# Performance work log

Measured on AMD Instinct MI355X. Metric: run time of the kernel, lower is better.

## Reference

```python
import jax, jax.numpy as jnp
import numpy as np

B, S, H, K, V = 1024, 50, 128, 4, 100000
ROUTING_TIMES = 3

def _squash(c):
    # c: [B,K,1,H]
    cap_norm = jnp.sum(jnp.square(c), -1, keepdims=True)
    scalar_factor = cap_norm / (1.0 + cap_norm) / jnp.sqrt(cap_norm + 1e-9)
    return scalar_factor * c

def setup_inputs() -> dict:
    key = jax.random.key(0)
    k1, k2, k3, k4, k5, k6 = jax.random.split(key, 6)
    item_seq = jax.random.randint(k1, (B, S), 0, V)
    mask = jax.random.randint(k2, (B, S), 0, 2).astype(jnp.float32)
    item = jax.random.randint(k3, (B, 1), 0, V)
    emb = jax.random.normal(k4, (V, H), dtype=jnp.float32) * 0.02
    W = jax.random.normal(k5, (H, H), dtype=jnp.float32) * (1.0 / np.sqrt(H))
    # bilinear_type==0 -> capsule routing logits initialized with randn
    capsule_weight0 = jax.random.normal(k6, (B, K, S), dtype=jnp.float32)
    return {"item_seq": item_seq, "mask": mask, "item": item,
            "emb": emb, "W": W, "capsule_weight0": capsule_weight0}

def reference(item_seq, mask, item, emb, W, capsule_weight0):
    # padding_idx=0: lookups see a zeroed row 0 (and get no grad there),
    # but calculate_loss uses the raw weight matrix.
    emb_lookup = emb.at[0].set(0.0)
    seq_emb = emb_lookup[item_seq]          # [B,S,H]
    item_e = emb_lookup[item[:, 0]]         # [B,H]  (squeeze(1))

    # CapsuleNetwork, bilinear_type==0: Linear(H,H,no bias) then repeat_interleave along hidden
    h = seq_emb @ W.T                        # [B,S,H]
    hat = jnp.repeat(h, K, axis=2)           # [B,S,H*K] (repeat_interleave semantics)
    hat = hat.reshape(B, S, K, H).transpose(0, 2, 1, 3)  # [B,K,S,H]
    hat_iter = jax.lax.stop_gradient(hat)    # stop_grad=True (detach)

    atten_mask = jnp.broadcast_to(mask[:, None, :], (B, K, S))
    cw = capsule_weight0
    cap = None
    for i in range(ROUTING_TIMES):
        # torch F.softmax with no dim on a 3-D tensor uses dim=0 (batch axis) -- faithful
        sw = jax.nn.softmax(cw, axis=0)
        sw = jnp.where(atten_mask == 0, 0.0, sw)[:, :, None, :]  # [B,K,1,S]
        src = hat_iter if i < ROUTING_TIMES - 1 else hat
        cap = _squash(sw @ src)                                   # [B,K,1,H]
        if i < ROUTING_TIMES - 1:
            delta = (hat_iter @ jnp.swapaxes(cap, 3, 2)).reshape(B, K, S)
            cw = cw + delta

    user_emb = cap.reshape(B, K, H)          # multi_interest_emb

    # hard readout: pick interest with max dot against target item
    cos = jnp.einsum('bkh,bh->bk', user_emb, item_e)
    k_index = jnp.argmax(cos, axis=1)        # [B]
    best = jnp.take_along_axis(user_emb, k_index[:, None, None], axis=1)[:, 0]  # [B,H]

    # cross-entropy over all items (raw embedding weight)
    scores = best @ emb.T                    # [B,V]
    logp = jax.nn.log_softmax(scores, axis=-1)
    loss = -jnp.mean(jnp.take_along_axis(logp, item, axis=1))
    return user_emb, loss
```

## Files before the change

kernel.cpp:

```cpp
#include <hip/hip_runtime.h>
#include <math.h>

#define BB 1024
#define SS 50
#define SSP 51
#define HH 128
#define KK 4
#define VV 100000
#define NVT 782
#define NVT8 784
#define KS (KK*SS)
#define NHM 400
#define NPAD_LAST 96.0f

typedef __attribute__((ext_vector_type(8))) short bf16x8;
typedef __attribute__((ext_vector_type(4))) float f32x4;

__device__ __forceinline__ ushort f2bf(float x) {
  unsigned u = __float_as_uint(x);
  unsigned r = u + 0x7FFF + ((u >> 16) & 1);
  return (ushort)(r >> 16);
}
__device__ __forceinline__ float bf2f(ushort u) {
  return __uint_as_float(((unsigned)u) << 16);
}
__device__ __forceinline__ bf16x8 cvt8(float4 a, float4 b) {
  bf16x8 r;
  r[0] = (short)f2bf(a.x); r[1] = (short)f2bf(a.y);
  r[2] = (short)f2bf(a.z); r[3] = (short)f2bf(a.w);
  r[4] = (short)f2bf(b.x); r[5] = (short)f2bf(b.y);
  r[6] = (short)f2bf(b.z); r[7] = (short)f2bf(b.w);
  return r;
}

__global__ __launch_bounds__(256) void k_pre(const float* __restrict__ emb,
                                             const float* __restrict__ cw0,
                                             float* __restrict__ cm,
                                             float* __restrict__ s1,
                                             float* __restrict__ s2,
                                             float* __restrict__ accum,
                                             const int* __restrict__ item_seq,
                                             const float* __restrict__ W,
                                             ushort* __restrict__ hb16) {
  const int t = threadIdx.x;
  if (blockIdx.x < NHM) {
    __shared__ __align__(16) ushort sWf[32 * 512];
    const int w = t >> 6;
    const int lane = t & 63;
    const int lr = lane & 15;
    const int lq = lane >> 4;
    const int m0 = blockIdx.x * 128;

#pragma unroll
    for (int it = 0; it < 8; ++it) {
      int pos = t + it * 256;
      int ch = pos >> 6, l = pos & 63;
      int n = (ch & 7) * 16 + (l & 15);
      int k0 = (ch >> 3) * 32 + (l >> 4) * 8;
      float4 a = *(const float4*)&W[n * HH + k0];
      float4 b = *(const float4*)&W[n * HH + k0 + 4];
      *(bf16x8*)&sWf[ch * 512 + l * 8] = cvt8(a, b);
    }

    bf16x8 af[4][2];
#pragma unroll
    for (int vv = 0; vv < 2; ++vv) {
      int m = m0 + w * 32 + vv * 16 + lr;
      int idx = item_seq[m];
#pragma unroll
      for (int ks = 0; ks < 4; ++ks) {
        if (idx != 0) {
          float4 a = *(const float4*)&emb[(size_t)idx * HH + ks * 32 + lq * 8];
          float4 b = *(const float4*)&emb[(size_t)idx * HH + ks * 32 + lq * 8 + 4];
          af[ks][vv] = cvt8(a, b);
        } else {
          af[ks][vv] = (bf16x8){0, 0, 0, 0, 0, 0, 0, 0};
        }
      }
    }
    __syncthreads();

    f32x4 acc[8][2];
#pragma unroll
    for (int nt = 0; nt < 8; ++nt)
#pragma unroll
      for (int vv = 0; vv < 2; ++vv) acc[nt][vv] = (f32x4){0.f, 0.f, 0.f, 0.f};

#pragma unroll
    for (int ks = 0; ks < 4; ++ks) {
      bf16x8 bw[8];
#pragma unroll
      for (int nt = 0; nt < 8; ++nt)
        bw[nt] = *(const bf16x8*)&sWf[(ks * 8 + nt) * 512 + lane * 8];
#pragma unroll
      for (int nt = 0; nt < 8; ++nt)
#pragma unroll
        for (int vv = 0; vv < 2; ++vv)
          acc[nt][vv] = __builtin_amdgcn_mfma_f32_16x16x32_bf16(af[ks][vv], bw[nt], acc[nt][vv], 0, 0, 0);
    }

#pragma unroll
    for (int nt = 0; nt < 8; ++nt)
#pragma unroll
      for (int vv = 0; vv < 2; ++vv)
#pragma unroll
        for (int r = 0; r < 4; ++r) {
          int m = m0 + w * 32 + vv * 16 + lq * 4 + r;
          hb16[(size_t)m * HH + nt * 16 + lr] = f2bf(acc[nt][vv][r]);
        }
  } else {
    __shared__ float red[256];
    const int c = blockIdx.x - NHM;
    if (t < 8) s1[t * KS + c] = 0.f;
    if (t >= 8 && t < 16) s2[(t - 8) * KS + c] = 0.f;
    if (c < 4) accum[c * 256 + t] = 0.f;
    float s = 0.f;
    for (int b = t; b < BB; b += 256) s += __expf(cw0[(size_t)b * KS + c]);
    red[t] = s;
    __syncthreads();
    for (int o = 128; o > 0; o >>= 1) {
      if (t < o) red[t] += red[t + o];
      __syncthreads();
    }
    if (t == 0) cm[c] = red[0];
  }
}

__global__ __launch_bounds__(256) void k_route(const float* __restrict__ cwsrc,
                                               float* __restrict__ cwdst,
                                               const ushort* __restrict__ hb16,
                                               const float* __restrict__ csum,
                                               int nslots,
                                               const float* __restrict__ mask,
                                               int last,
                                               float* __restrict__ out_ue,
                                               const float* __restrict__ emb,
                                               const int* __restrict__ item,
                                               ushort* __restrict__ bestb,
                                               float* __restrict__ csnext,
                                               float* __restrict__ si) {
  __shared__ ushort shT[128 * SSP];
  __shared__ float swl[KS];
  __shared__ float c32p[256];
  __shared__ float c32[128];
  __shared__ float csq[128];
  __shared__ float ie4r[32];
  __shared__ float ie4z[32];
  __shared__ float fac[4];
  __shared__ float cosk[4];
  __shared__ float cosr[4];
  __shared__ int kb;
  const int t = threadIdx.x;
  const int b = blockIdx.x;

  for (int p = t; p < (SS * HH) / 4; p += 256) {
    int flat = 4 * p;
    int s = flat >> 7, col = flat & 127;
    ushort4 v = *(const ushort4*)&hb16[(size_t)b * SS * HH + flat];
    shT[(col + 0) * SSP + s] = v.x;
    shT[(col + 1) * SSP + s] = v.y;
    shT[(col + 2) * SSP + s] = v.z;
    shT[(col + 3) * SSP + s] = v.w;
  }
  if (t < KS) {
    float den = 0.f;
    for (int g2 = 0; g2 < nslots; ++g2) den += csum[g2 * KS + t];
    float v = __expf(cwsrc[(size_t)b * KS + t]) / den;
    if (mask[b * SS + (t % SS)] == 0.0f) v = 0.0f;
    swl[t] = v;
  }
  __syncthreads();

  {
    int col = t & 127;
    int half = t >> 7;
    int k = col >> 5;
    float acc = 0.f;
    const float* swk = &swl[k * SS + half * 25];
    const ushort* hc = &shT[col * SSP + half * 25];
    for (int s = 0; s < 25; ++s) acc += swk[s] * bf2f(hc[s]);
    c32p[t] = acc;
  }
  __syncthreads();
  if (t < 128) c32[t] = c32p[t] + c32p[t + 128];
  __syncthreads();
  if (t < 4) {
    float nrm = 0.f;
#pragma unroll
    for (int j = 0; j < 32; ++j) { float c = c32[32 * t + j]; nrm += c * c; }
    nrm *= 4.0f;
    fac[t] = nrm / (1.0f + nrm) / sqrtf(nrm + 1e-9f);
  }
  __syncthreads();
  if (t < 128) csq[t] = c32[t] * fac[t >> 5];
  __syncthreads();

  if (!last) {
    if (t < KS) {
      int k = t / SS, s = t % SS;
      const float* cq = &csq[32 * k];
      float d = 0.f;
#pragma unroll
      for (int j = 0; j < 32; ++j) d += bf2f(shT[(32 * k + j) * SSP + s]) * cq[j];
      float nv = cwsrc[(size_t)b * KS + t] + 4.0f * d;
      cwdst[(size_t)b * KS + t] = nv;
      atomicAdd(&csnext[(b & 7) * KS + t], __expf(nv));
    }
  } else {
    for (int hh = t; hh < 512; hh += 256) {
      int k = hh >> 7, r = (hh & 127) >> 2;
      out_ue[(size_t)b * 512 + hh] = csq[32 * k + r];
    }
    if (t < 32) {
      int idx = item[b];
      const float* e = emb + (size_t)idx * HH + 4 * t;
      float v = e[0] + e[1] + e[2] + e[3];
      ie4r[t] = v;
      ie4z[t] = (idx == 0) ? 0.f : v;
    }
    __syncthreads();
    if (t < 4) {
      float cz = 0.f, cr = 0.f;
#pragma unroll
      for (int j = 0; j < 32; ++j) {
        cz += csq[32 * t + j] * ie4z[j];
        cr += csq[32 * t + j] * ie4r[j];
      }
      cosk[t] = cz; cosr[t] = cr;
    }
    __syncthreads();
    if (t == 0) {
      int kbest = 0; float bv = cosk[0];
#pragma unroll
      for (int k = 1; k < 4; ++k) if (cosk[k] > bv) { bv = cosk[k]; kbest = k; }
      kb = kbest;
      si[b] = cosr[kbest];
    }
    __syncthreads();
    if (t < 128) bestb[(size_t)b * HH + t] = f2bf(csq[32 * kb + (t >> 2)]);
  }
}

__global__ __launch_bounds__(256) void k_score_mfma(const ushort* __restrict__ bestb,
                                                    const float* __restrict__ emb,
                                                    float* __restrict__ accum) {
  const int lin = blockIdx.x;
  const int xcd = lin & 7;
  const int g = lin >> 3;
  const int bt8 = g & 7;
  const int vt = xcd * (NVT8 / 8) + (g >> 3);
  if (vt >= NVT) return;

  __shared__ __align__(16) ushort sB[32 * 512];
  __shared__ float ssm[128][4];
  const int t = threadIdx.x;
  const int w = t >> 6;
  const int lane = t & 63;
  const int lr = lane & 15;
  const int lq = lane >> 4;
  const int b0 = bt8 * 128;
  const int v0 = vt * 128 + w * 32;

  bf16x8 af[4][2];
#pragma unroll
  for (int vv = 0; vv < 2; ++vv) {
    int row = v0 + vv * 16 + lr;
    bool ok = row < VV;
    const float* er = emb + (size_t)row * HH;
#pragma unroll
    for (int ks = 0; ks < 4; ++ks) {
      if (ok) {
        float4 a = *(const float4*)&er[ks * 32 + lq * 8];
        float4 b = *(const float4*)&er[ks * 32 + lq * 8 + 4];
        af[ks][vv] = cvt8(a, b);
      } else {
        af[ks][vv] = (bf16x8){0, 0, 0, 0, 0, 0, 0, 0};
      }
    }
  }

#pragma unroll
  for (int it = 0; it < 8; ++it) {
    int pos = t + it * 256;
    int ch = pos >> 6;
    int l = pos & 63;
    int ks = ch >> 3, bt = ch & 7;
    *(bf16x8*)&sB[ch * 512 + l * 8] =
        *(const bf16x8*)&bestb[(size_t)(b0 + bt * 16 + (l & 15)) * HH + ks * 32 + (l >> 4) * 8];
  }

  f32x4 acc[8][2];
#pragma unroll
  for (int bt = 0; bt < 8; ++bt)
#pragma unroll
    for (int vv = 0; vv < 2; ++vv) acc[bt][vv] = (f32x4){0.f, 0.f, 0.f, 0.f};

  __syncthreads();

  bf16x8 bcur[8];
#pragma unroll
  for (int bt = 0; bt < 8; ++bt)
    bcur[bt] = *(const bf16x8*)&sB[bt * 512 + lane * 8];

#pragma unroll
  for (int ks = 0; ks < 4; ++ks) {
    bf16x8 bnxt[8];
    if (ks < 3) {
#pragma unroll
      for (int bt = 0; bt < 8; ++bt)
        bnxt[bt] = *(const bf16x8*)&sB[((ks + 1) * 8 + bt) * 512 + lane * 8];
    }
#pragma unroll
    for (int bt = 0; bt < 8; ++bt)
#pragma unroll
      for (int vv = 0; vv < 2; ++vv)
        acc[bt][vv] = __builtin_amdgcn_mfma_f32_16x16x32_bf16(af[ks][vv], bcur[bt], acc[bt][vv], 0, 0, 0);
    if (ks < 3) {
#pragma unroll
      for (int bt = 0; bt < 8; ++bt) bcur[bt] = bnxt[bt];
    }
  }

#pragma unroll
  for (int bt = 0; bt < 8; ++bt) {
    float s = 0.f;
#pragma unroll
    for (int vv = 0; vv < 2; ++vv)
#pragma unroll
      for (int r = 0; r < 4; ++r) s += __expf(acc[bt][vv][r]);
    s += __shfl_xor(s, 16);
    s += __shfl_xor(s, 32);
    if (lq == 0) ssm[bt * 16 + lr][w] = s;
  }
  __syncthreads();
  if (t < 128) {
    float s = ssm[t][0] + ssm[t][1] + ssm[t][2] + ssm[t][3];
    atomicAdd(&accum[b0 + t], s);
  }
}

__global__ __launch_bounds__(256) void k_loss(const float* __restrict__ accum,
                                              const float* __restrict__ si,
                                              float* __restrict__ outloss) {
  __shared__ float red[256];
  const int t = threadIdx.x;
  float s = 0.f;
  for (int b = t; b < BB; b += 256)
    s += logf(accum[b] - NPAD_LAST) - si[b];
  red[t] = s;
  __syncthreads();
  for (int o = 128; o > 0; o >>= 1) {
    if (t < o) red[t] += red[t + o];
    __syncthreads();
  }
  if (t == 0) outloss[0] = red[0] / (float)BB;
}

extern "C" void kernel_launch(void* const* d_in, const int* in_sizes, int n_in,
                              void* d_out, int out_size, void* d_ws, size_t ws_size,
                              hipStream_t stream) {
  const int*   item_seq = (const int*)d_in[0];
  const float* mask     = (const float*)d_in[1];
  const int*   item     = (const int*)d_in[2];
  const float* emb      = (const float*)d_in[3];
  const float* W        = (const float*)d_in[4];
  const float* cw0      = (const float*)d_in[5];
  float* out = (float*)d_out;
  float* outloss = out + (size_t)BB * KK * HH;

  float* ws = (float*)d_ws;
  float* cm    = ws;
  float* s1    = cm + 256;
  float* s2    = s1 + 8 * KS;
  float* si    = s2 + 8 * KS;
  float* accum = si + BB;
  float* cw    = accum + BB;
  ushort* hb16  = (ushort*)(cw + (size_t)BB * KS);
  ushort* bestb = hb16 + (size_t)BB * SS * HH;

  k_pre<<<dim3(NHM + KS), 256, 0, stream>>>(emb, cw0, cm, s1, s2, accum,
                                            item_seq, W, hb16);

  k_route<<<dim3(BB), 256, 0, stream>>>(cw0, cw, hb16, cm, 1, mask, 0, out, emb, item, bestb, s1, si);
  k_route<<<dim3(BB), 256, 0, stream>>>(cw, cw, hb16, s1, 8, mask, 0, out, emb, item, bestb, s2, si);
  k_route<<<dim3(BB), 256, 0, stream>>>(cw, cw, hb16, s2, 8, mask, 1, out, emb, item, bestb, s1, si);

  k_score_mfma<<<dim3(NVT8 * 8), 256, 0, stream>>>(bestb, emb, accum);
  k_loss<<<dim3(1), 256, 0, stream>>>(accum, si, outloss);
}
```

Before: 215.9 us.

## Pre-convert embedding table to bf16 and process two vocab tiles per block

Adds a kernel that converts the full fp32 embedding table to a padded bf16 copy once per call. The scoring kernel then loads bf16 rows directly and each block covers 256 vocab rows in two halves, reusing its staged bestb tile in shared memory. This halves the emb reads in scoring and the number of bestb staging loads, and drops per-block conversion and bounds checks. In exchange it adds an extra full pass over emb (fp32 read plus bf16 write) and a larger workspace.

Result: slower. 229.6 us (+6.3%).

```diff
diff --git a/kernel.cpp b/kernel.cpp
--- a/kernel.cpp
+++ b/kernel.cpp
@@ -9,6 +9,8 @@
 #define VV 100000
 #define NVT 782
 #define NVT8 784
+#define NSV 392
+#define VPAD (NVT8*128)
 #define KS (KK*SS)
 #define NHM 400
 #define NPAD_LAST 96.0f
@@ -31,6 +33,19 @@
   r[4] = (short)f2bf(b.x); r[5] = (short)f2bf(b.y);
   r[6] = (short)f2bf(b.z); r[7] = (short)f2bf(b.w);
   return r;
+}
+
+__global__ __launch_bounds__(256) void k_conv(const float* __restrict__ emb,
+                                              ushort* __restrict__ embb) {
+  size_t i = ((size_t)blockIdx.x * 256 + threadIdx.x) * 4;
+  ushort4 o;
+  if (i < (size_t)VV * HH) {
+    float4 v = *(const float4*)&emb[i];
+    o = make_ushort4(f2bf(v.x), f2bf(v.y), f2bf(v.z), f2bf(v.w));
+  } else {
+    o = make_ushort4(0, 0, 0, 0);
+  }
+  *(ushort4*)&embb[i] = o;
 }
 
 __global__ __launch_bounds__(256) void k_pre(const float* __restrict__ emb,
@@ -242,14 +257,16 @@
 }
 
 __global__ __launch_bounds__(256) void k_score_mfma(const ushort* __restrict__ bestb,
-                                                    const float* __restrict__ emb,
+                                                    const ushort* __restrict__ embb,
                                                     float* __restrict__ accum) {
   const int lin = blockIdx.x;
   const int xcd = lin & 7;
   const int g = lin >> 3;
   const int bt8 = g & 7;
-  const int vt = xcd * (NVT8 / 8) + (g >> 3);
-  if (vt >= NVT) return;
+  const int sv = xcd * (NSV / 8) + (g >> 3);
+  if (sv >= NSV - 1) return;
+  const int b0 = bt8 * 128;
+  const int vbase = sv * 256;
 
   __shared__ __align__(16) ushort sB[32 * 512];
   __shared__ float ssm[128][4];
@@ -258,26 +275,6 @@
   const int lane = t & 63;
   const int lr = lane & 15;
   const int lq = lane >> 4;
-  const int b0 = bt8 * 128;
-  const int v0 = vt * 128 + w * 32;
-
-  bf16x8 af[4][2];
-#pragma unroll
-  for (int vv = 0; vv < 2; ++vv) {
-    int row = v0 + vv * 16 + lr;
-    bool ok = row < VV;
-    const float* er = emb + (size_t)row * HH;
-#pragma unroll
-    for (int ks = 0; ks < 4; ++ks) {
-      if (ok) {
-        float4 a = *(const float4*)&er[ks * 32 + lq * 8];
-        float4 b = *(const float4*)&er[ks * 32 + lq * 8 + 4];
-        af[ks][vv] = cvt8(a, b);
-      } else {
-        af[ks][vv] = (bf16x8){0, 0, 0, 0, 0, 0, 0, 0};
-      }
-    }
-  }
 
 #pragma unroll
   for (int it = 0; it < 8; ++it) {
@@ -288,46 +285,64 @@
     *(bf16x8*)&sB[ch * 512 + l * 8] =
         *(const bf16x8*)&bestb[(size_t)(b0 + bt * 16 + (l & 15)) * HH + ks * 32 + (l >> 4) * 8];
   }
-
-  f32x4 acc[8][2];
-#pragma unroll
-  for (int bt = 0; bt < 8; ++bt)
-#pragma unroll
-    for (int vv = 0; vv < 2; ++vv) acc[bt][vv] = (f32x4){0.f, 0.f, 0.f, 0.f};
-
-  __syncthreads();
-
-  bf16x8 bcur[8];
-#pragma unroll
-  for (int bt = 0; bt < 8; ++bt)
-    bcur[bt] = *(const bf16x8*)&sB[bt * 512 + lane * 8];
-
-#pragma unroll
-  for (int ks = 0; ks < 4; ++ks) {
-    bf16x8 bnxt[8];
-    if (ks < 3) {
+  __syncthreads();
+
+  float sacc[8];
+#pragma unroll
+  for (int bt = 0; bt < 8; ++bt) sacc[bt] = 0.f;
+
+  for (int vh = 0; vh < 2; ++vh) {
+    const int v0 = vbase + vh * 128 + w * 32;
+
+    bf16x8 af[4][2];
+#pragma unroll
+    for (int ks = 0; ks < 4; ++ks)
+#pragma unroll
+      for (int vv = 0; vv < 2; ++vv)
+        af[ks][vv] = *(const bf16x8*)&embb[(size_t)(v0 + vv * 16 + lr) * HH + ks * 32 + lq * 8];
+
+    f32x4 acc[8][2];
+#pragma unroll
+    for (int bt = 0; bt < 8; ++bt)
+#pragma unroll
+      for (int vv = 0; vv < 2; ++vv) acc[bt][vv] = (f32x4){0.f, 0.f, 0.f, 0.f};
+
+    bf16x8 bcur[8];
+#pragma unroll
+    for (int bt = 0; bt < 8; ++bt)
+      bcur[bt] = *(const bf16x8*)&sB[bt * 512 + lane * 8];
+
+#pragma unroll
+    for (int ks = 0; ks < 4; ++ks) {
+      bf16x8 bnxt[8];
+      if (ks < 3) {
+#pragma unroll
+        for (int bt = 0; bt < 8; ++bt)
+          bnxt[bt] = *(const bf16x8*)&sB[((ks + 1) * 8 + bt) * 512 + lane * 8];
+      }
 #pragma unroll
       for (int bt = 0; bt < 8; ++bt)
-        bnxt[bt] = *(const bf16x8*)&sB[((ks + 1) * 8 + bt) * 512 + lane * 8];
-    }
-#pragma unroll
-    for (int bt = 0; bt < 8; ++bt)
+#pragma unroll
+        for (int vv = 0; vv < 2; ++vv)
+          acc[bt][vv] = __builtin_amdgcn_mfma_f32_16x16x32_bf16(af[ks][vv], bcur[bt], acc[bt][vv], 0, 0, 0);
+      if (ks < 3) {
+#pragma unroll
+        for (int bt = 0; bt < 8; ++bt) bcur[bt] = bnxt[bt];
+      }
+    }
+
+#pragma unroll
+    for (int bt = 0; bt < 8; ++bt) {
 #pragma unroll
       for (int vv = 0; vv < 2; ++vv)
-        acc[bt][vv] = __builtin_amdgcn_mfma_f32_16x16x32_bf16(af[ks][vv], bcur[bt], acc[bt][vv], 0, 0, 0);
-    if (ks < 3) {
-#pragma unroll
-      for (int bt = 0; bt < 8; ++bt) bcur[bt] = bnxt[bt];
+#pragma unroll
+        for (int r = 0; r < 4; ++r) sacc[bt] += __expf(acc[bt][vv][r]);
     }
   }
 
 #pragma unroll
   for (int bt = 0; bt < 8; ++bt) {
-    float s = 0.f;
-#pragma unroll
-    for (int vv = 0; vv < 2; ++vv)
-#pragma unroll
-      for (int r = 0; r < 4; ++r) s += __expf(acc[bt][vv][r]);
+    float s = sacc[bt];
     s += __shfl_xor(s, 16);
     s += __shfl_xor(s, 32);
     if (lq == 0) ssm[bt * 16 + lr][w] = s;
@@ -376,15 +391,17 @@
   float* accum = si + BB;
   float* cw    = accum + BB;
   ushort* hb16  = (ushort*)(cw + (size_t)BB * KS);
-  ushort* bestb = hb16 + (size_t)BB * SS * HH;
+  ushort* embb  = hb16 + (size_t)BB * SS * HH;
+  ushort* bestb = embb + (size_t)VPAD * HH;
 
   k_pre<<<dim3(NHM + KS), 256, 0, stream>>>(emb, cw0, cm, s1, s2, accum,
                                             item_seq, W, hb16);
+  k_conv<<<dim3((VPAD * HH) / 1024), 256, 0, stream>>>(emb, embb);
 
   k_route<<<dim3(BB), 256, 0, stream>>>(cw0, cw, hb16, cm, 1, mask, 0, out, emb, item, bestb, s1, si);
   k_route<<<dim3(BB), 256, 0, stream>>>(cw, cw, hb16, s1, 8, mask, 0, out, emb, item, bestb, s2, si);
   k_route<<<dim3(BB), 256, 0, stream>>>(cw, cw, hb16, s2, 8, mask, 1, out, emb, item, bestb, s1, si);
 
-  k_score_mfma<<<dim3(NVT8 * 8), 256, 0, stream>>>(bestb, emb, accum);
+  k_score_mfma<<<dim3(NSV * 8), 256, 0, stream>>>(bestb, embb, accum);
   k_loss<<<dim3(1), 256, 0, stream>>>(accum, si, outloss);
 }
```
